# Kernel tuning notes

Hardware: AMD Instinct MI355X
Metric: run time of the kernel (lower is better)

## Reference

```python
import jax, jax.numpy as jnp
import numpy as np

EMBED_DIM = 1024
NUM_HEADS = 16
HEAD_DIM = EMBED_DIM // NUM_HEADS
BATCH = 2
SEQ = 2048


def setup_inputs() -> dict:
    key = jax.random.key(0)
    ks = jax.random.split(key, 9)
    s = EMBED_DIM ** -0.5
    inp = {"x": jax.random.normal(ks[0], (BATCH, SEQ, EMBED_DIM), dtype=jnp.float32)}
    names = ["Wq", "Wk", "Wv", "Wo"]
    for i, n in enumerate(names):
        inp[n] = jax.random.normal(ks[1 + i], (EMBED_DIM, EMBED_DIM), dtype=jnp.float32) * s
        inp["b" + n[1]] = jax.random.normal(ks[5 + i], (EMBED_DIM,), dtype=jnp.float32) * 0.02
    return inp


def reference(x, Wq, bq, Wk, bk, Wv, bv, Wo, bo):
    B, S, E = x.shape
    H, D = NUM_HEADS, HEAD_DIM
    scaling = D ** -0.5
    # projections (torch Linear: x @ W.T + b), reshape to (B, H, S, D)
    q = (x @ Wq.T + bq).reshape(B, S, H, D).transpose(0, 2, 1, 3)
    k = (x @ Wk.T + bk).reshape(B, S, H, D).transpose(0, 2, 1, 3)
    v = (x @ Wv.T + bv).reshape(B, S, H, D).transpose(0, 2, 1, 3)
    # full materialized score matrix, matching the original module
    scores = jnp.einsum("bhqd,bhkd->bhqk", q, k) * scaling
    causal = jnp.triu(jnp.ones((S, S), dtype=bool), k=1)  # True above diagonal
    scores = jnp.where(causal[None, None], -jnp.inf, scores)
    attn = jax.nn.softmax(scores, axis=-1)
    out = jnp.einsum("bhqk,bhkd->bhqd", attn, v)  # (B, H, S, D)
    out = out.transpose(0, 2, 1, 3).reshape(B, S, E)
    return out @ Wo.T + bo
```

## Files before the change

### kernel.cpp

```cpp
#include <hip/hip_runtime.h>
#include <stdint.h>

typedef __bf16 bf16;
typedef __bf16 bf16x8 __attribute__((ext_vector_type(8)));
typedef __bf16 bf16x4 __attribute__((ext_vector_type(4)));
typedef float  f32x4  __attribute__((ext_vector_type(4)));

#define E_DIM 1024
#define S_LEN 2048
#define BATCH 2
#define NH 16
#define DH 64

#define NEG_INF (-__builtin_inff())

__device__ __forceinline__ void load_lds16(const bf16* g, bf16* l) {
    __builtin_amdgcn_global_load_lds(
        (const __attribute__((address_space(1))) void*)g,
        (__attribute__((address_space(3))) void*)l, 16, 0, 0);
}

__global__ __launch_bounds__(256) void convert_kernel(
    const float* __restrict__ s0, const float* __restrict__ s1,
    const float* __restrict__ s2, const float* __restrict__ s3,
    const float* __restrict__ s4,
    bf16* __restrict__ d0, bf16* __restrict__ d1, bf16* __restrict__ d2,
    bf16* __restrict__ d3, bf16* __restrict__ d4,
    int n0, int n1)
{
    const float* src; bf16* dst; int n;
    switch (blockIdx.y) {
        case 0:  src = s0; dst = d0; n = n0; break;
        case 1:  src = s1; dst = d1; n = n1; break;
        case 2:  src = s2; dst = d2; n = n1; break;
        case 3:  src = s3; dst = d3; n = n1; break;
        default: src = s4; dst = d4; n = n1; break;
    }
    int i = (blockIdx.x * 256 + threadIdx.x) * 4;
    if (i >= n) return;
    float4 v = *(const float4*)(src + i);
    bf16x4 o;
    o[0] = (bf16)v.x; o[1] = (bf16)v.y; o[2] = (bf16)v.z; o[3] = (bf16)v.w;
    *(bf16x4*)(dst + i) = o;
}

__global__ __launch_bounds__(256) void gemm_kernel(
    const bf16* __restrict__ A,
    const bf16* __restrict__ W0, const bf16* __restrict__ W1, const bf16* __restrict__ W2,
    const float* __restrict__ bias0, const float* __restrict__ bias1, const float* __restrict__ bias2,
    bf16* __restrict__ outQ, bf16* __restrict__ outK, bf16* __restrict__ outVt,
    float* __restrict__ outF, int final_mode)
{
    __shared__ bf16 As0[128 * 32], As1[128 * 32];
    __shared__ bf16 Bs0[128 * 32], Bs1[128 * 32];

    int mode;
    const bf16* W; const float* bias;
    if (final_mode) { mode = 3; W = W0; bias = bias0; }
    else {
        mode = blockIdx.z;
        W    = (mode == 0) ? W0 : (mode == 1 ? W1 : W2);
        bias = (mode == 0) ? bias0 : (mode == 1 ? bias1 : bias2);
    }

    const int bm = blockIdx.y * 128, bn = blockIdx.x * 128;
    const int t = threadIdx.x;
    const int lane = t & 63, w = t >> 6;
    const int quad = lane >> 4, l16 = lane & 15;
    const int wm = (w & 1) * 64, wn = (w >> 1) * 64;

    const int r0 = w * 16;
    const int srow = r0 + (lane >> 2), scol = (lane & 3) * 8;
    const bf16* Ag0 = A + (size_t)(bm + srow) * E_DIM + scol;
    const bf16* Ag1 = Ag0 + (size_t)64 * E_DIM;
    const bf16* Wg0 = W + (size_t)(bn + srow) * E_DIM + scol;
    const bf16* Wg1 = Wg0 + (size_t)64 * E_DIM;
    bf16* a00 = As0 + r0 * 32;  bf16* a01 = As0 + (64 + r0) * 32;
    bf16* a10 = As1 + r0 * 32;  bf16* a11 = As1 + (64 + r0) * 32;
    bf16* b00 = Bs0 + r0 * 32;  bf16* b01 = Bs0 + (64 + r0) * 32;
    bf16* b10 = Bs1 + r0 * 32;  bf16* b11 = Bs1 + (64 + r0) * 32;

    f32x4 acc[4][4];
#pragma unroll
    for (int i = 0; i < 4; i++)
#pragma unroll
        for (int j = 0; j < 4; j++) acc[i][j] = f32x4{0.f, 0.f, 0.f, 0.f};

    for (int kt = 0; kt < E_DIM; kt += 64) {
        __syncthreads();
        load_lds16(Ag0 + kt,      a00);
        load_lds16(Ag1 + kt,      a01);
        load_lds16(Ag0 + kt + 32, a10);
        load_lds16(Ag1 + kt + 32, a11);
        load_lds16(Wg0 + kt,      b00);
        load_lds16(Wg1 + kt,      b01);
        load_lds16(Wg0 + kt + 32, b10);
        load_lds16(Wg1 + kt + 32, b11);
        __syncthreads();

#pragma unroll
        for (int half = 0; half < 2; half++) {
            const bf16* Asx = half ? As1 : As0;
            const bf16* Bsx = half ? Bs1 : Bs0;
            bf16x8 af[4], bfr[4];
#pragma unroll
            for (int i = 0; i < 4; i++)
                af[i] = *(const bf16x8*)(Asx + (wm + i * 16 + l16) * 32 + quad * 8);
#pragma unroll
            for (int j = 0; j < 4; j++)
                bfr[j] = *(const bf16x8*)(Bsx + (wn + j * 16 + l16) * 32 + quad * 8);
#pragma unroll
            for (int i = 0; i < 4; i++)
#pragma unroll
                for (int j = 0; j < 4; j++)
                    acc[i][j] = __builtin_amdgcn_mfma_f32_16x16x32_bf16(af[i], bfr[j], acc[i][j], 0, 0, 0);
        }
    }

#pragma unroll
    for (int j = 0; j < 4; j++) {
        const int n = bn + wn + j * 16 + l16;
        const float bv = bias[n];
#pragma unroll
        for (int i = 0; i < 4; i++) {
            const int m0 = bm + wm + i * 16 + quad * 4;
            if (mode == 3) {
#pragma unroll
                for (int r = 0; r < 4; r++)
                    outF[(size_t)(m0 + r) * E_DIM + n] = acc[i][j][r] + bv;
            } else if (mode == 2) {
                const int b_ = m0 >> 11, s0 = m0 & (S_LEN - 1);
                const int h = n >> 6, d = n & 63;
                bf16x4 pv;
#pragma unroll
                for (int r = 0; r < 4; r++) pv[r] = (bf16)(acc[i][j][r] + bv);
                *(bf16x4*)(outVt + ((size_t)((b_ * NH + h) * DH + d)) * S_LEN + s0) = pv;
            } else {
                bf16* o = (mode == 0) ? outQ : outK;
                const float sc = (mode == 0) ? 0.125f : 1.0f;
                const int h = n >> 6, d = n & 63;
#pragma unroll
                for (int r = 0; r < 4; r++) {
                    const int m = m0 + r;
                    const int b_ = m >> 11, s = m & (S_LEN - 1);
                    o[((size_t)(b_ * NH + h) * S_LEN + s) * DH + d] = (bf16)((acc[i][j][r] + bv) * sc);
                }
            }
        }
    }
}

__global__ __launch_bounds__(256, 1) void attn_kernel(
    const bf16* __restrict__ Qb, const bf16* __restrict__ Kb,
    const bf16* __restrict__ Vtb, bf16* __restrict__ Ob)
{
    __shared__ bf16 Ks[128 * 72];
    __shared__ bf16 Vs[64 * 136];
    __shared__ bf16 Ps[4][32 * 136];

    const int t = threadIdx.x, lane = t & 63, w = t >> 6;
    const int quad = lane >> 4, l16 = lane & 15;

    const int i = blockIdx.x;
    const int xcd = i & 7, rr = i >> 3;
    const int bh = (xcd << 2) | (rr & 3);
    const int pr = rr >> 2;
    const int qlo = pr, qhi = 15 - pr;

    const bf16* Qg = Qb + (size_t)bh * S_LEN * DH;
    const bf16* Kg = Kb + (size_t)bh * S_LEN * DH;
    const bf16* Vg = Vtb + (size_t)bh * DH * S_LEN;
    const int b_ = bh >> 4, h = bh & 15;
    bf16* Og = Ob + (size_t)b_ * S_LEN * E_DIM + h * DH;

    bf16* Pw = Ps[w];
    const int inrow0 = w * 32;

    bf16x8 aq[2][2][2];
#pragma unroll
    for (int qt = 0; qt < 2; qt++) {
        const int qrow0 = (qt ? qhi : qlo) * 128 + inrow0;
#pragma unroll
        for (int st = 0; st < 2; st++) {
            const bf16* qp = Qg + (size_t)(qrow0 + st * 16 + l16) * DH + quad * 8;
            aq[qt][st][0] = *(const bf16x8*)(qp);
            aq[qt][st][1] = *(const bf16x8*)(qp + 32);
        }
    }

    f32x4 o[2][2][4];
    float l_part[2][2][4];
#pragma unroll
    for (int qt = 0; qt < 2; qt++)
#pragma unroll
        for (int st = 0; st < 2; st++)
#pragma unroll
            for (int dt = 0; dt < 4; dt++) {
                o[qt][st][dt] = f32x4{0.f, 0.f, 0.f, 0.f};
                l_part[qt][st][dt] = 0.f;
            }

    const int T = qhi + 1;
    const int krow = t >> 3, kcol8 = (t & 7) * 8;
    const int vrow = t >> 4, vcol8 = (t & 15) * 8;

    uint4 kc[4], vc[4];
#pragma unroll
    for (int k = 0; k < 4; k++)
        kc[k] = *(const uint4*)(Kg + (size_t)(krow + 32 * k) * DH + kcol8);
#pragma unroll
    for (int k = 0; k < 4; k++)
        vc[k] = *(const uint4*)(Vg + (size_t)(vrow + 16 * k) * S_LEN + vcol8);

    for (int kt = 0; kt < T; kt++) {
        __syncthreads();
#pragma unroll
        for (int k = 0; k < 4; k++)
            *(uint4*)(Ks + (krow + 32 * k) * 72 + kcol8) = kc[k];
#pragma unroll
        for (int k = 0; k < 4; k++)
            *(uint4*)(Vs + (vrow + 16 * k) * 136 + vcol8) = vc[k];
        __syncthreads();

        if (kt + 1 < T) {
            const int nb = (kt + 1) * 128;
#pragma unroll
            for (int k = 0; k < 4; k++)
                kc[k] = *(const uint4*)(Kg + (size_t)(nb + krow + 32 * k) * DH + kcol8);
#pragma unroll
            for (int k = 0; k < 4; k++)
                vc[k] = *(const uint4*)(Vg + (size_t)(vrow + 16 * k) * S_LEN + nb + vcol8);
        }

#pragma unroll
        for (int qt = 0; qt < 2; qt++) {
            if (qt == 0 && kt > qlo) continue;
            const bool diag = qt ? (kt == qhi) : (kt == qlo);

            f32x4 sv[2][8];
#pragma unroll
            for (int jt = 0; jt < 8; jt++) {
                const bf16* kp = Ks + (jt * 16 + l16) * 72 + quad * 8;
                bf16x8 bk0 = *(const bf16x8*)(kp);
                bf16x8 bk1 = *(const bf16x8*)(kp + 32);
#pragma unroll
                for (int st = 0; st < 2; st++) {
                    f32x4 s = f32x4{0.f, 0.f, 0.f, 0.f};
                    s = __builtin_amdgcn_mfma_f32_16x16x32_bf16(aq[qt][st][0], bk0, s, 0, 0, 0);
                    s = __builtin_amdgcn_mfma_f32_16x16x32_bf16(aq[qt][st][1], bk1, s, 0, 0, 0);
                    sv[st][jt] = s;
                }
            }

            if (diag) {
#pragma unroll
                for (int st = 0; st < 2; st++) {
                    const int inrow_base = inrow0 + st * 16 + quad * 4;
#pragma unroll
                    for (int jt = 0; jt < 8; jt++) {
                        const int kcol = jt * 16 + l16;
#pragma unroll
                        for (int r = 0; r < 4; r++)
                            if (kcol > inrow_base + r) sv[st][jt][r] = NEG_INF;
                    }
                }
            }

#pragma unroll
            for (int st = 0; st < 2; st++)
#pragma unroll
                for (int jt = 0; jt < 8; jt++)
#pragma unroll
                    for (int r = 0; r < 4; r++) {
                        const float pe = __expf(sv[st][jt][r]);
                        sv[st][jt][r] = pe;
                        l_part[qt][st][r] += pe;
                    }

#pragma unroll
            for (int st = 0; st < 2; st++)
#pragma unroll
                for (int jt = 0; jt < 8; jt++)
#pragma unroll
                    for (int r = 0; r < 4; r++)
                        Pw[(st * 16 + quad * 4 + r) * 136 + jt * 16 + l16] = (bf16)sv[st][jt][r];

#pragma unroll
            for (int ks = 0; ks < 4; ks++) {
                bf16x8 ap0 = *(const bf16x8*)(Pw + l16 * 136 + ks * 32 + quad * 8);
                bf16x8 ap1 = *(const bf16x8*)(Pw + (16 + l16) * 136 + ks * 32 + quad * 8);
#pragma unroll
                for (int dt = 0; dt < 4; dt++) {
                    bf16x8 bv = *(const bf16x8*)(Vs + (dt * 16 + l16) * 136 + ks * 32 + quad * 8);
                    o[qt][0][dt] = __builtin_amdgcn_mfma_f32_16x16x32_bf16(ap0, bv, o[qt][0][dt], 0, 0, 0);
                    o[qt][1][dt] = __builtin_amdgcn_mfma_f32_16x16x32_bf16(ap1, bv, o[qt][1][dt], 0, 0, 0);
                }
            }
        }
    }

#pragma unroll
    for (int qt = 0; qt < 2; qt++) {
        const int qrow0 = (qt ? qhi : qlo) * 128 + inrow0;
#pragma unroll
        for (int st = 0; st < 2; st++) {
#pragma unroll
            for (int r = 0; r < 4; r++) {
                float l = l_part[qt][st][r];
                l += __shfl_xor(l, 1);
                l += __shfl_xor(l, 2);
                l += __shfl_xor(l, 4);
                l += __shfl_xor(l, 8);
                l_part[qt][st][r] = 1.0f / l;
            }
#pragma unroll
            for (int r = 0; r < 4; r++) {
                const int srow = qrow0 + st * 16 + quad * 4 + r;
#pragma unroll
                for (int dt = 0; dt < 4; dt++)
                    Og[(size_t)srow * E_DIM + dt * 16 + l16] =
                        (bf16)(o[qt][st][dt][r] * l_part[qt][st][r]);
            }
        }
    }
}

extern "C" void kernel_launch(void* const* d_in, const int* in_sizes, int n_in,
                              void* d_out, int out_size, void* d_ws, size_t ws_size,
                              hipStream_t stream)
{
    const float* x  = (const float*)d_in[0];
    const float* Wq = (const float*)d_in[1];
    const float* bq = (const float*)d_in[2];
    const float* Wk = (const float*)d_in[3];
    const float* bk = (const float*)d_in[4];
    const float* Wv = (const float*)d_in[5];
    const float* bv = (const float*)d_in[6];
    const float* Wo = (const float*)d_in[7];
    const float* bo = (const float*)d_in[8];
    float* out = (float*)d_out;

    char* ws = (char*)d_ws;
    const size_t MB = 1ull << 20;
    bf16* xb  = (bf16*)(ws + 0);
    bf16* wqb = (bf16*)(ws + 8 * MB);
    bf16* wkb = (bf16*)(ws + 10 * MB);
    bf16* wvb = (bf16*)(ws + 12 * MB);
    bf16* wob = (bf16*)(ws + 14 * MB);
    bf16* Qb  = (bf16*)(ws + 16 * MB);
    bf16* Kb  = (bf16*)(ws + 24 * MB);
    bf16* Vtb = (bf16*)(ws + 32 * MB);
    bf16* Ab  = (bf16*)(ws + 40 * MB);

    convert_kernel<<<dim3(4096, 5), 256, 0, stream>>>(
        x, Wq, Wk, Wv, Wo, xb, wqb, wkb, wvb, wob, 4194304, 1048576);

    gemm_kernel<<<dim3(8, 32, 3), 256, 0, stream>>>(
        xb, wqb, wkb, wvb, bq, bk, bv, Qb, Kb, Vtb, nullptr, 0);

    attn_kernel<<<dim3(256), 256, 0, stream>>>(Qb, Kb, Vtb, Ab);

    gemm_kernel<<<dim3(8, 32, 1), 256, 0, stream>>>(
        Ab, wob, wob, wob, bo, bo, bo, nullptr, nullptr, nullptr, out, 1);
}
```

Baseline: 237.6 us.

## Halve attention query tile to 64 rows and double grid to 512 blocks

The attention kernel now gives each block two 64-row query tiles (paired low/high for causal balance) instead of two 128-row tiles, with each wave owning 16 rows rather than 32. The grid doubles to 512 blocks and the single-block-per-CU launch bound is dropped, aiming for more parallelism across CUs and lower register pressure. In exchange each K/V tile loaded into LDS is reused by fewer query rows, so global and LDS traffic per FLOP rises.

```diff
diff --git a/kernel.cpp b/kernel.cpp
--- a/kernel.cpp
+++ b/kernel.cpp
@@ -150,13 +150,13 @@
     }
 }
 
-__global__ __launch_bounds__(256, 1) void attn_kernel(
+__global__ __launch_bounds__(256) void attn_kernel(
     const bf16* __restrict__ Qb, const bf16* __restrict__ Kb,
     const bf16* __restrict__ Vtb, bf16* __restrict__ Ob)
 {
     __shared__ bf16 Ks[128 * 72];
     __shared__ bf16 Vs[64 * 136];
-    __shared__ bf16 Ps[4][32 * 136];
+    __shared__ bf16 Ps[4][16 * 136];
 
     const int t = threadIdx.x, lane = t & 63, w = t >> 6;
     const int quad = lane >> 4, l16 = lane & 15;
@@ -165,7 +165,7 @@
     const int xcd = i & 7, rr = i >> 3;
     const int bh = (xcd << 2) | (rr & 3);
     const int pr = rr >> 2;
-    const int qlo = pr, qhi = 15 - pr;
+    const int qtl = pr, qth = 31 - pr;
 
     const bf16* Qg = Qb + (size_t)bh * S_LEN * DH;
     const bf16* Kg = Kb + (size_t)bh * S_LEN * DH;
@@ -174,33 +174,28 @@
     bf16* Og = Ob + (size_t)b_ * S_LEN * E_DIM + h * DH;
 
     bf16* Pw = Ps[w];
-    const int inrow0 = w * 32;
-
-    bf16x8 aq[2][2][2];
+
+    bf16x8 aq[2][2];
 #pragma unroll
     for (int qt = 0; qt < 2; qt++) {
-        const int qrow0 = (qt ? qhi : qlo) * 128 + inrow0;
-#pragma unroll
-        for (int st = 0; st < 2; st++) {
-            const bf16* qp = Qg + (size_t)(qrow0 + st * 16 + l16) * DH + quad * 8;
-            aq[qt][st][0] = *(const bf16x8*)(qp);
-            aq[qt][st][1] = *(const bf16x8*)(qp + 32);
-        }
-    }
-
-    f32x4 o[2][2][4];
-    float l_part[2][2][4];
+        const int qrow0 = (qt ? qth : qtl) * 64 + w * 16;
+        const bf16* qp = Qg + (size_t)(qrow0 + l16) * DH + quad * 8;
+        aq[qt][0] = *(const bf16x8*)(qp);
+        aq[qt][1] = *(const bf16x8*)(qp + 32);
+    }
+
+    f32x4 o[2][4];
+    float l_part[2][4];
 #pragma unroll
     for (int qt = 0; qt < 2; qt++)
 #pragma unroll
-        for (int st = 0; st < 2; st++)
-#pragma unroll
-            for (int dt = 0; dt < 4; dt++) {
-                o[qt][st][dt] = f32x4{0.f, 0.f, 0.f, 0.f};
-                l_part[qt][st][dt] = 0.f;
-            }
-
-    const int T = qhi + 1;
+        for (int dt = 0; dt < 4; dt++) {
+            o[qt][dt] = f32x4{0.f, 0.f, 0.f, 0.f};
+            l_part[qt][dt] = 0.f;
+        }
+
+    const int nkt_lo = (qtl >> 1) + 1;
+    const int T = (qth >> 1) + 1;
     const int krow = t >> 3, kcol8 = (t & 7) * 8;
     const int vrow = t >> 4, vcol8 = (t & 15) * 8;
 
@@ -234,93 +229,79 @@
 
 #pragma unroll
         for (int qt = 0; qt < 2; qt++) {
-            if (qt == 0 && kt > qlo) continue;
-            const bool diag = qt ? (kt == qhi) : (kt == qlo);
-
-            f32x4 sv[2][8];
+            if (qt == 0 && kt >= nkt_lo) continue;
+            const int qtile = qt ? qth : qtl;
+            const bool diag = (kt == (qtile >> 1));
+
+            f32x4 sv[8];
 #pragma unroll
             for (int jt = 0; jt < 8; jt++) {
                 const bf16* kp = Ks + (jt * 16 + l16) * 72 + quad * 8;
                 bf16x8 bk0 = *(const bf16x8*)(kp);
                 bf16x8 bk1 = *(const bf16x8*)(kp + 32);
-#pragma unroll
-                for (int st = 0; st < 2; st++) {
-                    f32x4 s = f32x4{0.f, 0.f, 0.f, 0.f};
-                    s = __builtin_amdgcn_mfma_f32_16x16x32_bf16(aq[qt][st][0], bk0, s, 0, 0, 0);
-                    s = __builtin_amdgcn_mfma_f32_16x16x32_bf16(aq[qt][st][1], bk1, s, 0, 0, 0);
-                    sv[st][jt] = s;
+                f32x4 s = f32x4{0.f, 0.f, 0.f, 0.f};
+                s = __builtin_amdgcn_mfma_f32_16x16x32_bf16(aq[qt][0], bk0, s, 0, 0, 0);
+                s = __builtin_amdgcn_mfma_f32_16x16x32_bf16(aq[qt][1], bk1, s, 0, 0, 0);
+                sv[jt] = s;
+            }
+
+            if (diag) {
+                const int inrow_base = 64 * (qtile & 1) + w * 16 + quad * 4;
+#pragma unroll
+                for (int jt = 0; jt < 8; jt++) {
+                    const int kcol = jt * 16 + l16;
+#pragma unroll
+                    for (int r = 0; r < 4; r++)
+                        if (kcol > inrow_base + r) sv[jt][r] = NEG_INF;
                 }
             }
 
-            if (diag) {
-#pragma unroll
-                for (int st = 0; st < 2; st++) {
-                    const int inrow_base = inrow0 + st * 16 + quad * 4;
-#pragma unroll
-                    for (int jt = 0; jt < 8; jt++) {
-                        const int kcol = jt * 16 + l16;
-#pragma unroll
-                        for (int r = 0; r < 4; r++)
-                            if (kcol > inrow_base + r) sv[st][jt][r] = NEG_INF;
-                    }
+#pragma unroll
+            for (int jt = 0; jt < 8; jt++)
+#pragma unroll
+                for (int r = 0; r < 4; r++) {
+                    const float pe = __expf(sv[jt][r]);
+                    sv[jt][r] = pe;
+                    l_part[qt][r] += pe;
+                }
+
+#pragma unroll
+            for (int jt = 0; jt < 8; jt++)
+#pragma unroll
+                for (int r = 0; r < 4; r++)
+                    Pw[(quad * 4 + r) * 136 + jt * 16 + l16] = (bf16)sv[jt][r];
+
+#pragma unroll
+            for (int ks = 0; ks < 4; ks++) {
+                bf16x8 ap = *(const bf16x8*)(Pw + l16 * 136 + ks * 32 + quad * 8);
+#pragma unroll
+                for (int dt = 0; dt < 4; dt++) {
+                    bf16x8 bv = *(const bf16x8*)(Vs + (dt * 16 + l16) * 136 + ks * 32 + quad * 8);
+                    o[qt][dt] = __builtin_amdgcn_mfma_f32_16x16x32_bf16(ap, bv, o[qt][dt], 0, 0, 0);
                 }
             }
-
-#pragma unroll
-            for (int st = 0; st < 2; st++)
-#pragma unroll
-                for (int jt = 0; jt < 8; jt++)
-#pragma unroll
-                    for (int r = 0; r < 4; r++) {
-                        const float pe = __expf(sv[st][jt][r]);
-                        sv[st][jt][r] = pe;
-                        l_part[qt][st][r] += pe;
-                    }
-
-#pragma unroll
-            for (int st = 0; st < 2; st++)
-#pragma unroll
-                for (int jt = 0; jt < 8; jt++)
-#pragma unroll
-                    for (int r = 0; r < 4; r++)
-                        Pw[(st * 16 + quad * 4 + r) * 136 + jt * 16 + l16] = (bf16)sv[st][jt][r];
-
-#pragma unroll
-            for (int ks = 0; ks < 4; ks++) {
-                bf16x8 ap0 = *(const bf16x8*)(Pw + l16 * 136 + ks * 32 + quad * 8);
-                bf16x8 ap1 = *(const bf16x8*)(Pw + (16 + l16) * 136 + ks * 32 + quad * 8);
-#pragma unroll
-                for (int dt = 0; dt < 4; dt++) {
-                    bf16x8 bv = *(const bf16x8*)(Vs + (dt * 16 + l16) * 136 + ks * 32 + quad * 8);
-                    o[qt][0][dt] = __builtin_amdgcn_mfma_f32_16x16x32_bf16(ap0, bv, o[qt][0][dt], 0, 0, 0);
-                    o[qt][1][dt] = __builtin_amdgcn_mfma_f32_16x16x32_bf16(ap1, bv, o[qt][1][dt], 0, 0, 0);
-                }
-            }
         }
     }
 
 #pragma unroll
     for (int qt = 0; qt < 2; qt++) {
-        const int qrow0 = (qt ? qhi : qlo) * 128 + inrow0;
-#pragma unroll
-        for (int st = 0; st < 2; st++) {
-#pragma unroll
-            for (int r = 0; r < 4; r++) {
-                float l = l_part[qt][st][r];
-                l += __shfl_xor(l, 1);
-                l += __shfl_xor(l, 2);
-                l += __shfl_xor(l, 4);
-                l += __shfl_xor(l, 8);
-                l_part[qt][st][r] = 1.0f / l;
-            }
-#pragma unroll
-            for (int r = 0; r < 4; r++) {
-                const int srow = qrow0 + st * 16 + quad * 4 + r;
-#pragma unroll
-                for (int dt = 0; dt < 4; dt++)
-                    Og[(size_t)srow * E_DIM + dt * 16 + l16] =
-                        (bf16)(o[qt][st][dt][r] * l_part[qt][st][r]);
-            }
+        const int qrow0 = (qt ? qth : qtl) * 64 + w * 16;
+#pragma unroll
+        for (int r = 0; r < 4; r++) {
+            float l = l_part[qt][r];
+            l += __shfl_xor(l, 1);
+            l += __shfl_xor(l, 2);
+            l += __shfl_xor(l, 4);
+            l += __shfl_xor(l, 8);
+            l_part[qt][r] = 1.0f / l;
+        }
+#pragma unroll
+        for (int r = 0; r < 4; r++) {
+            const int srow = qrow0 + quad * 4 + r;
+#pragma unroll
+            for (int dt = 0; dt < 4; dt++)
+                Og[(size_t)srow * E_DIM + dt * 16 + l16] =
+                    (bf16)(o[qt][dt][r] * l_part[qt][r]);
         }
     }
 }
@@ -358,7 +339,7 @@
     gemm_kernel<<<dim3(8, 32, 3), 256, 0, stream>>>(
         xb, wqb, wkb, wvb, bq, bk, bv, Qb, Kb, Vtb, nullptr, 0);
 
-    attn_kernel<<<dim3(256), 256, 0, stream>>>(Qb, Kb, Vtb, Ab);
+    attn_kernel<<<dim3(512), 256, 0, stream>>>(Qb, Kb, Vtb, Ab);
 
     gemm_kernel<<<dim3(8, 32, 1), 256, 0, stream>>>(
         Ab, wob, wob, wob, bo, bo, bo, nullptr, nullptr, nullptr, out, 1);
```

After: 241.9 us. No clear change (+1.8%).

## Double-buffer GEMM LDS tiles to overlap global loads with MFMA compute

Applied to the files above, without the earlier changes.

Restructures the projection GEMM main loop into a two-stage ping-pong pipeline. The first K-slice is prefetched before the loop, and each iteration issues the direct-to-LDS loads for the next 32-wide slice before running the MFMAs on the current one, with one barrier per iteration instead of two. The aim is to hide global-to-LDS load latency behind matrix compute. In exchange the K-step shrinks from 64 to 32, so there are twice as many barriers and less MFMA work per barrier, and correctness relies on the barrier draining the outstanding async LDS loads.

```diff
diff --git a/kernel.cpp b/kernel.cpp
--- a/kernel.cpp
+++ b/kernel.cpp
@@ -51,8 +51,8 @@
     bf16* __restrict__ outQ, bf16* __restrict__ outK, bf16* __restrict__ outVt,
     float* __restrict__ outF, int final_mode)
 {
-    __shared__ bf16 As0[128 * 32], As1[128 * 32];
-    __shared__ bf16 Bs0[128 * 32], Bs1[128 * 32];
+    __shared__ bf16 As[2][128 * 32];
+    __shared__ bf16 Bs[2][128 * 32];
 
     int mode;
     const bf16* W; const float* bias;
@@ -75,10 +75,6 @@
     const bf16* Ag1 = Ag0 + (size_t)64 * E_DIM;
     const bf16* Wg0 = W + (size_t)(bn + srow) * E_DIM + scol;
     const bf16* Wg1 = Wg0 + (size_t)64 * E_DIM;
-    bf16* a00 = As0 + r0 * 32;  bf16* a01 = As0 + (64 + r0) * 32;
-    bf16* a10 = As1 + r0 * 32;  bf16* a11 = As1 + (64 + r0) * 32;
-    bf16* b00 = Bs0 + r0 * 32;  bf16* b01 = Bs0 + (64 + r0) * 32;
-    bf16* b10 = Bs1 + r0 * 32;  bf16* b11 = Bs1 + (64 + r0) * 32;
 
     f32x4 acc[4][4];
 #pragma unroll
@@ -86,35 +82,37 @@
 #pragma unroll
         for (int j = 0; j < 4; j++) acc[i][j] = f32x4{0.f, 0.f, 0.f, 0.f};
 
-    for (int kt = 0; kt < E_DIM; kt += 64) {
+    load_lds16(Ag0, As[0] + r0 * 32);
+    load_lds16(Ag1, As[0] + (64 + r0) * 32);
+    load_lds16(Wg0, Bs[0] + r0 * 32);
+    load_lds16(Wg1, Bs[0] + (64 + r0) * 32);
+
+    int cur = 0;
+    for (int kt = 0; kt < E_DIM; kt += 32) {
         __syncthreads();
-        load_lds16(Ag0 + kt,      a00);
-        load_lds16(Ag1 + kt,      a01);
-        load_lds16(Ag0 + kt + 32, a10);
-        load_lds16(Ag1 + kt + 32, a11);
-        load_lds16(Wg0 + kt,      b00);
-        load_lds16(Wg1 + kt,      b01);
-        load_lds16(Wg0 + kt + 32, b10);
-        load_lds16(Wg1 + kt + 32, b11);
-        __syncthreads();
-
-#pragma unroll
-        for (int half = 0; half < 2; half++) {
-            const bf16* Asx = half ? As1 : As0;
-            const bf16* Bsx = half ? Bs1 : Bs0;
-            bf16x8 af[4], bfr[4];
-#pragma unroll
-            for (int i = 0; i < 4; i++)
-                af[i] = *(const bf16x8*)(Asx + (wm + i * 16 + l16) * 32 + quad * 8);
+
+        if (kt + 32 < E_DIM) {
+            const int nxt = cur ^ 1;
+            load_lds16(Ag0 + kt + 32, As[nxt] + r0 * 32);
+            load_lds16(Ag1 + kt + 32, As[nxt] + (64 + r0) * 32);
+            load_lds16(Wg0 + kt + 32, Bs[nxt] + r0 * 32);
+            load_lds16(Wg1 + kt + 32, Bs[nxt] + (64 + r0) * 32);
+        }
+
+        bf16x8 af[4], bfr[4];
+#pragma unroll
+        for (int i = 0; i < 4; i++)
+            af[i] = *(const bf16x8*)(As[cur] + (wm + i * 16 + l16) * 32 + quad * 8);
+#pragma unroll
+        for (int j = 0; j < 4; j++)
+            bfr[j] = *(const bf16x8*)(Bs[cur] + (wn + j * 16 + l16) * 32 + quad * 8);
+#pragma unroll
+        for (int i = 0; i < 4; i++)
 #pragma unroll
             for (int j = 0; j < 4; j++)
-                bfr[j] = *(const bf16x8*)(Bsx + (wn + j * 16 + l16) * 32 + quad * 8);
-#pragma unroll
-            for (int i = 0; i < 4; i++)
-#pragma unroll
-                for (int j = 0; j < 4; j++)
-                    acc[i][j] = __builtin_amdgcn_mfma_f32_16x16x32_bf16(af[i], bfr[j], acc[i][j], 0, 0, 0);
-        }
+                acc[i][j] = __builtin_amdgcn_mfma_f32_16x16x32_bf16(af[i], bfr[j], acc[i][j], 0, 0, 0);
+
+        cur ^= 1;
     }
 
 #pragma unroll
```

Result: faster. 232.2 us (-2.3%).
